# Optimization experiments

Measured on AMD Instinct MI355X. Metric: run time of the kernel, lower is better.

## Reference

```python
import jax, jax.numpy as jnp
import numpy as np

B, T, C = 2, 2048, 2048
NH, NKV = 16, 4
HD = C // NH  # 128
DFF = 4 * C


def rmsnorm(x):
    eps = jnp.finfo(x.dtype).eps
    return x * jax.lax.rsqrt(jnp.mean(jnp.square(x), axis=-1, keepdims=True) + eps)


def rotary(x, cos, sin):
    # x: [B,T,H,HD], cos/sin: [1,T,1,HD//2]
    d = x.shape[-1] // 2
    x1, x2 = x[..., :d], x[..., d:]
    return jnp.concatenate([x1 * cos + x2 * sin, -x1 * sin + x2 * cos], axis=-1)


def setup_inputs() -> dict:
    key = jax.random.key(0)
    ks = jax.random.split(key, 8)
    x = jax.random.normal(ks[0], (B, T, C), jnp.float32)
    inv_freq = 1.0 / (10000.0 ** (jnp.arange(HD // 2, dtype=jnp.float32) / (HD // 2)))
    ang = jnp.arange(T, dtype=jnp.float32)[:, None] * inv_freq[None, :]  # [T, HD//2]
    cos = jnp.cos(ang)[None, :, None, :]
    sin = jnp.sin(ang)[None, :, None, :]
    s = 0.02
    wq = jax.random.normal(ks[1], (C, NH * HD), jnp.float32) * s
    wk = jax.random.normal(ks[2], (C, NKV * HD), jnp.float32) * s
    wv = jax.random.normal(ks[3], (C, NKV * HD), jnp.float32) * s
    wo = jax.random.normal(ks[4], (C, C), jnp.float32) * s
    w_fc = jax.random.normal(ks[5], (C, DFF), jnp.float32) * s
    w_proj = jax.random.normal(ks[6], (DFF, C), jnp.float32) * s
    return {"x": x, "cos": cos, "sin": sin, "wq": wq, "wk": wk, "wv": wv,
            "wo": wo, "w_fc": w_fc, "w_proj": w_proj}


def reference(x, cos, sin, wq, wk, wv, wo, w_fc, w_proj):
    # --- attention sublayer (pre-norm residual) ---
    h = rmsnorm(x)
    q = (h @ wq).reshape(B, T, NH, HD)
    k = (h @ wk).reshape(B, T, NKV, HD)
    v = (h @ wv).reshape(B, T, NKV, HD)
    q = rmsnorm(rotary(q, cos, sin))
    k = rmsnorm(rotary(k, cos, sin))
    rep = NH // NKV
    k = jnp.repeat(k, rep, axis=2)  # [B,T,NH,HD]
    v = jnp.repeat(v, rep, axis=2)
    scale = 1.0 / np.sqrt(HD)
    scores = jnp.einsum('bqhd,bkhd->bhqk', q, k) * scale
    causal = jnp.tril(jnp.ones((T, T), dtype=bool))
    scores = jnp.where(causal[None, None], scores, jnp.finfo(scores.dtype).min)
    attn = jax.nn.softmax(scores, axis=-1)
    y = jnp.einsum('bhqk,bkhd->bqhd', attn, v).reshape(B, T, C)
    x = x + y @ wo
    # --- MLP sublayer (relu^2) ---
    h = rmsnorm(x)
    h = jnp.square(jax.nn.relu(h @ w_fc))
    x = x + h @ w_proj
    return x
```

## Files before the change

kernel.cpp:

```cpp
#include <hip/hip_runtime.h>
#include <cstdint>
#include <cstddef>


#define B_    2
#define T_    2048
#define C_    2048
#define NH_   16
#define NKV_  4
#define HD_   128
#define DFF_  8192
#define EPS_  1.1920928955078125e-07f

typedef short          bf16x8 __attribute__((ext_vector_type(8)));
typedef float          f32x4  __attribute__((ext_vector_type(4)));
typedef unsigned short u16;
typedef unsigned short u16x8  __attribute__((ext_vector_type(8)));
typedef unsigned short u16x4  __attribute__((ext_vector_type(4)));

__device__ __forceinline__ u16 f2bf(float f) {
    unsigned u = __float_as_uint(f);
    unsigned r = u + 0x7fffu + ((u >> 16) & 1u);
    return (u16)(r >> 16);
}
__device__ __forceinline__ float bf2f(u16 u) {
    return __uint_as_float((unsigned)u << 16);
}

__device__ __forceinline__ void load_lds16(const void* g, void* l) {
    __builtin_amdgcn_global_load_lds(
        (__attribute__((address_space(1))) void*)(g),
        (__attribute__((address_space(3))) void*)(l), 16, 0, 0);
}

__device__ __forceinline__ unsigned lds_addr(const void* p) {
    return (unsigned)(unsigned long long)(__attribute__((address_space(3))) const void*)p;
}

struct TD  { const float* src; u16* dst; int K, N, boff; };
struct TD6 { TD t[6]; };

#define TRBLKS_ 10752

__global__ void prep_all(TD6 d, const float* __restrict__ x, u16* __restrict__ hout) {
    __shared__ u16 tile[32][136];
    __shared__ float part[4];
    int bid = blockIdx.x;
    int tid = threadIdx.x;

    if (bid >= TRBLKS_) {
        int row = bid - TRBLKS_;
        const float4* xr = (const float4*)(x + (size_t)row * C_);
        float4 a = xr[tid];
        float4 b = xr[tid + 256];
        float ss = a.x * a.x + a.y * a.y + a.z * a.z + a.w * a.w
                 + b.x * b.x + b.y * b.y + b.z * b.z + b.w * b.w;
        for (int m = 1; m < 64; m <<= 1) ss += __shfl_xor(ss, m, 64);
        if ((tid & 63) == 0) part[tid >> 6] = ss;
        __syncthreads();
        float tot = part[0] + part[1] + part[2] + part[3];
        float sc = rsqrtf(tot * (1.0f / C_) + EPS_);
        u16x4 o1, o2;
        o1[0] = f2bf(a.x * sc); o1[1] = f2bf(a.y * sc); o1[2] = f2bf(a.z * sc); o1[3] = f2bf(a.w * sc);
        o2[0] = f2bf(b.x * sc); o2[1] = f2bf(b.y * sc); o2[2] = f2bf(b.z * sc); o2[3] = f2bf(b.w * sc);
        u16x4* orow = (u16x4*)(hout + (size_t)row * C_);
        orow[tid]       = o1;
        orow[tid + 256] = o2;
        return;
    }

    int di = 0;
    for (int i = 5; i > 0; --i) if (bid >= d.t[i].boff) { di = i; break; }
    const float* src = d.t[di].src;
    u16* dst = d.t[di].dst;
    int K = d.t[di].K, N = d.t[di].N;
    int lb = bid - d.t[di].boff;
    int nx = N >> 5;
    int n0 = (lb % nx) * 32;
    int k0 = (lb / nx) * 128;

    int kr = tid >> 3;
    int nc = (tid & 7) * 4;
    for (int r = 0; r < 4; ++r) {
        int kk = kr + r * 32;
        float4 v = *(const float4*)&src[(size_t)(k0 + kk) * N + n0 + nc];
        tile[nc + 0][kk] = f2bf(v.x);
        tile[nc + 1][kk] = f2bf(v.y);
        tile[nc + 2][kk] = f2bf(v.z);
        tile[nc + 3][kk] = f2bf(v.w);
    }
    __syncthreads();
    int nL = tid >> 4;
    int kc = (tid & 15) * 8;
    for (int w2 = 0; w2 < 2; ++w2) {
        int n = nL + w2 * 16;
        u16x8 o = *(const u16x8*)&tile[n][kc];
        *(u16x8*)&dst[(size_t)(n0 + n) * K + k0 + kc] = o;
    }
}

#define TVB_ 1024

__global__ void rope_tv(const float* __restrict__ Xq, const float* __restrict__ Xk,
                        const float* __restrict__ cosb, const float* __restrict__ sinb,
                        u16* __restrict__ Oq, u16* __restrict__ Ok,
                        const u16* __restrict__ vb, u16* __restrict__ Vt) {
    int bid = blockIdx.x;
    if (bid < TVB_) {
        int bxx  = bid & 127;
        int kvh  = (bid >> 7) & 3;
        int b    = bid >> 9;
        int dblk = bxx & 1;
        int t0   = (bxx >> 1) * 32;
        int dl   = threadIdx.x & 63;
        int tc   = threadIdx.x >> 6;
        int d    = dblk * 64 + dl;
        u16x8 v8;
        for (int j = 0; j < 8; ++j) {
            int t = t0 + tc * 8 + j;
            v8[j] = vb[((size_t)(b * T_ + t) * NKV_ + kvh) * HD_ + d];
        }
        *(u16x8*)(Vt + ((size_t)((b * NKV_ + kvh) * HD_ + d)) * T_ + t0 + tc * 8) = v8;
        return;
    }
    int gw   = (int)(((bid - TVB_) * blockDim.x + threadIdx.x) >> 6);
    int lane = threadIdx.x & 63;
    const float* X; u16* O; int t;
    if (gw < B_ * T_ * NH_) {
        X = Xq + (size_t)gw * HD_;  O = Oq + (size_t)gw * HD_;  t = (gw / NH_) % T_;
    } else {
        int w2 = gw - B_ * T_ * NH_;
        X = Xk + (size_t)w2 * HD_;  O = Ok + (size_t)w2 * HD_;  t = (w2 / NKV_) % T_;
    }
    float x1 = X[lane];
    float x2 = X[64 + lane];
    float c  = cosb[t * 64 + lane];
    float sn = sinb[t * 64 + lane];
    float r1 = x1 * c + x2 * sn;
    float r2 = x2 * c - x1 * sn;
    float ss = r1 * r1 + r2 * r2;
    for (int m = 1; m < 64; m <<= 1) ss += __shfl_xor(ss, m, 64);
    float sc = rsqrtf(ss * (1.0f / HD_) + EPS_);
    O[lane]      = f2bf(r1 * sc);
    O[64 + lane] = f2bf(r2 * sc);
}

__global__ void reduce_rms(const float* __restrict__ x, const u16* __restrict__ p0,
                           const u16* __restrict__ p1, float* __restrict__ x2,
                           u16* __restrict__ hout) {
    int row = blockIdx.x;
    const float4* xr = (const float4*)(x + (size_t)row * C_);
    const u16x4* a0 = (const u16x4*)(p0 + (size_t)row * C_);
    const u16x4* a1 = (const u16x4*)(p1 + (size_t)row * C_);
    float4 v[2];
    float ss = 0.f;
    for (int h = 0; h < 2; ++h) {
        int idx = threadIdx.x + h * 256;
        float4 xv = xr[idx];
        u16x4 b0 = a0[idx], b1 = a1[idx];
        v[h].x = xv.x + bf2f(b0[0]) + bf2f(b1[0]);
        v[h].y = xv.y + bf2f(b0[1]) + bf2f(b1[1]);
        v[h].z = xv.z + bf2f(b0[2]) + bf2f(b1[2]);
        v[h].w = xv.w + bf2f(b0[3]) + bf2f(b1[3]);
        ss += v[h].x * v[h].x + v[h].y * v[h].y + v[h].z * v[h].z + v[h].w * v[h].w;
    }
    for (int m = 1; m < 64; m <<= 1) ss += __shfl_xor(ss, m, 64);
    __shared__ float part[4];
    if ((threadIdx.x & 63) == 0) part[threadIdx.x >> 6] = ss;
    __syncthreads();
    float tot = part[0] + part[1] + part[2] + part[3];
    float sc = rsqrtf(tot * (1.0f / C_) + EPS_);
    float4* x2r = (float4*)(x2 + (size_t)row * C_);
    u16x4* hr   = (u16x4*)(hout + (size_t)row * C_);
    for (int h = 0; h < 2; ++h) {
        int idx = threadIdx.x + h * 256;
        x2r[idx] = v[h];
        u16x4 o;
        o[0] = f2bf(v[h].x * sc); o[1] = f2bf(v[h].y * sc);
        o[2] = f2bf(v[h].z * sc); o[3] = f2bf(v[h].w * sc);
        hr[idx] = o;
    }
}

__global__ void reduce_out(const float* __restrict__ x2, const u16* __restrict__ p0,
                           const u16* __restrict__ p1, float* __restrict__ out) {
    size_t i = (size_t)blockIdx.x * 256 + threadIdx.x;
    float4 xv = ((const float4*)x2)[i];
    u16x4 b0 = ((const u16x4*)p0)[i];
    u16x4 b1 = ((const u16x4*)p1)[i];
    float4 o;
    o.x = xv.x + bf2f(b0[0]) + bf2f(b1[0]);
    o.y = xv.y + bf2f(b0[1]) + bf2f(b1[1]);
    o.z = xv.z + bf2f(b0[2]) + bf2f(b1[2]);
    o.w = xv.w + bf2f(b0[3]) + bf2f(b1[3]);
    ((float4*)out)[i] = o;
}


#define BARRIER() do { __builtin_amdgcn_s_barrier();                     \
                       asm volatile("" ::: "memory"); } while (0)
#define LGKMN(N)  do { asm volatile("s_waitcnt lgkmcnt(" #N ")" ::: "memory");\
                       __builtin_amdgcn_sched_barrier(0); } while (0)

#define DSR(dst, base, lit)                                              \
    asm volatile("ds_read_b128 %0, %1 offset:" lit : "=v"(dst) : "v"(base))

#define READ_AFL() do {                                                  \
    DSR(afl[0][0], aB0, "0");     DSR(afl[0][1], aB1, "0");              \
    DSR(afl[1][0], aB0, "2048");  DSR(afl[1][1], aB1, "2048");           \
    DSR(afl[2][0], aB0, "4096");  DSR(afl[2][1], aB1, "4096");           \
    DSR(afl[3][0], aB0, "6144");  DSR(afl[3][1], aB1, "6144"); } while (0)

#define READ_AFH() do {                                                  \
    DSR(afh[0][0], aB0, "8192");  DSR(afh[0][1], aB1, "8192");           \
    DSR(afh[1][0], aB0, "10240"); DSR(afh[1][1], aB1, "10240");          \
    DSR(afh[2][0], aB0, "12288"); DSR(afh[2][1], aB1, "12288");          \
    DSR(afh[3][0], aB0, "14336"); DSR(afh[3][1], aB1, "14336"); } while (0)

#define READ_BL() do {                                                   \
    DSR(bl[0][0], bB0, "0");     DSR(bl[0][1], bB1, "0");                \
    DSR(bl[1][0], bB0, "2048");  DSR(bl[1][1], bB1, "2048"); } while (0)

#define READ_BH() do {                                                   \
    DSR(bh[0][0], bB0, "4096");  DSR(bh[0][1], bB1, "4096");             \
    DSR(bh[1][0], bB0, "6144");  DSR(bh[1][1], bB1, "6144"); } while (0)

#define MFMA_BLK(AF, BF, MB, NB)                                             \
    _Pragma("unroll")                                                        \
    for (int ks = 0; ks < 2; ++ks)                                           \
        _Pragma("unroll")                                                    \
        for (int mi = 0; mi < 4; ++mi)                                       \
            _Pragma("unroll")                                                \
            for (int ni = 0; ni < 2; ++ni)                                   \
                acc[MB + mi][NB + ni] =                                      \
                    __builtin_amdgcn_mfma_f32_16x16x32_bf16(                 \
                        AF[mi][ks], BF[ni][ks], acc[MB + mi][NB + ni], 0, 0, 0);

template <int EPI>
__launch_bounds__(512, 1)
__global__ void gemm256(const u16* __restrict__ A, const u16* __restrict__ Bt,
                        void* __restrict__ out, void* __restrict__ out2,
                        void* __restrict__ out3, int M, int N, int K, int Ks) {
    __shared__ __attribute__((aligned(16))) u16 sh[65536];

    int tid  = threadIdx.x;
    int l    = tid & 63;
    int w    = tid >> 6;
    int l16  = l & 15;
    int quad = l >> 4;
    int sw   = l & 7;
    int wm   = w >> 2, wn = w & 3;

    int nwg = gridDim.x * gridDim.y;
    int id  = blockIdx.y * gridDim.x + blockIdx.x;
    int cpx = nwg >> 3;
    int sid = (id & 7) * cpx + (id >> 3);
    int GN   = (cpx >= 64) ? 8 : 4;
    int span = gridDim.y * GN;
    int bnb  = sid / span;
    int r0   = sid % span;
    int bm   = r0 / GN;
    int bn   = bnb * GN + (r0 % GN);

    size_t koff = (size_t)blockIdx.z * K;
    int nt = K >> 6;

    int csrc = ((l & 7) ^ ((l >> 3) & 7)) * 8;
    int srow = w * 8 + (l >> 3);
    const u16* Ast = A  + (size_t)(bm * 256 + srow) * Ks + koff + csrc;
    const u16* Bst = Bt + (size_t)(bn * 256 + srow) * Ks + koff + csrc;

    auto stageA = [&](int h, int kk, int buf) {
        const u16* g = Ast + (size_t)(h * 128) * Ks + kk;
        u16* d = sh + buf * 32768 + h * 8192 + w * 512;
        load_lds16(g, d);
        load_lds16(g + (size_t)64 * Ks, d + 4096);
    };
    auto stageB = [&](int h, int kk, int buf) {
        const u16* g = Bst + (size_t)(h * 128) * Ks + kk;
        u16* d = sh + buf * 32768 + (2 + h) * 8192 + w * 512;
        load_lds16(g, d);
        load_lds16(g + (size_t)64 * Ks, d + 4096);
    };

    f32x4 acc[8][4];
#pragma unroll
    for (int m = 0; m < 8; ++m)
#pragma unroll
        for (int n = 0; n < 4; ++n) acc[m][n] = (f32x4){0.f, 0.f, 0.f, 0.f};

    stageB(0, 0, 0); stageA(0, 0, 0); stageA(1, 0, 0); stageB(1, 0, 0);
    stageB(0, 64, 1); stageA(0, 64, 1);
    asm volatile("s_waitcnt vmcnt(4)" ::: "memory");
    BARRIER();

    bf16x8 afl[4][2], afh[4][2], bl[2][2], bh[2][2];
    unsigned shbase = lds_addr(sh);
    unsigned ck0 = (unsigned)((quad ^ sw) * 16);
    unsigned ck1 = ck0 ^ 64u;
    unsigned Aoff = (unsigned)(wm * 16384 + l16 * 128);
    unsigned Boff = (unsigned)((2 + (wn >> 1)) * 16384 + (wn & 1) * 8192
                               + l16 * 128);
    unsigned aB0c = shbase + Aoff + ck0, aB1c = shbase + Aoff + ck1;
    unsigned bB0c = shbase + Boff + ck0, bB1c = shbase + Boff + ck1;

    for (int t = 0; t < nt; ++t) {
        int buf = t & 1;
        unsigned bo  = (unsigned)buf << 16;
        unsigned aB0 = aB0c + bo, aB1 = aB1c + bo;
        unsigned bB0 = bB0c + bo, bB1 = bB1c + bo;
        bool s1 = (t + 1 < nt), s2 = (t + 2 < nt);

        READ_AFL();
        READ_BL();
        READ_BH();
        READ_AFH();
        if (s1) { stageA(1, (t + 1) * 64, buf ^ 1);
                  stageB(1, (t + 1) * 64, buf ^ 1); }

        LGKMN(12);
        __builtin_amdgcn_s_setprio(1);
        MFMA_BLK(afl, bl, 0, 0);
        __builtin_amdgcn_s_setprio(0);

        LGKMN(8);
        __builtin_amdgcn_s_setprio(1);
        MFMA_BLK(afl, bh, 0, 2);
        __builtin_amdgcn_s_setprio(0);

        LGKMN(0);
        BARRIER();
        if (s2) { stageB(0, (t + 2) * 64, buf);
                  stageA(0, (t + 2) * 64, buf); }

        __builtin_amdgcn_s_setprio(1);
        MFMA_BLK(afh, bl, 4, 0);
        MFMA_BLK(afh, bh, 4, 2);
        __builtin_amdgcn_s_setprio(0);

        if (s2)      asm volatile("s_waitcnt vmcnt(4)" ::: "memory");
        else if (s1) asm volatile("s_waitcnt vmcnt(0)" ::: "memory");
        BARRIER();
    }

#pragma unroll
    for (int m = 0; m < 8; ++m)
#pragma unroll
        for (int n = 0; n < 4; ++n)
#pragma unroll
            for (int r = 0; r < 4; ++r) {
                int rg = bm * 256 + wm * 128 + m * 16 + quad * 4 + r;
                int cg = bn * 256 + wn * 64 + n * 16 + l16;
                float v = acc[m][n][r];
                if (EPI == 2) {
                    float tv = fmaxf(v, 0.f);
                    ((u16*)out)[(size_t)rg * N + cg] = f2bf(tv * tv);
                } else if (EPI == 4) {
                    if (cg < 2048)      ((float*)out)[(size_t)rg * 2048 + cg] = v;
                    else if (cg < 2560) ((float*)out2)[(size_t)rg * 512 + (cg - 2048)] = v;
                    else                ((u16*)out3)[(size_t)rg * 512 + (cg - 2560)] = f2bf(v);
                } else {
                    u16* p = (blockIdx.z == 0) ? (u16*)out : (u16*)out2;
                    p[(size_t)rg * N + cg] = f2bf(v);
                }
            }
}

__launch_bounds__(256, 2)
__global__ void flash_attn2(const u16* __restrict__ Q, const u16* __restrict__ Kb,
                            const u16* __restrict__ Vt, u16* __restrict__ Y) {
    __shared__ __attribute__((aligned(16))) u16 Qs[128 * 128];
    __shared__ __attribute__((aligned(16))) u16 Ks[64 * 128];
    __shared__ __attribute__((aligned(16))) u16 Vs[2][128 * 64];

    int bid = blockIdx.x;
    int half = bid >> 8, idx = bid & 255;
    int qr = idx & 15;
    int qt = half ? (15 - qr) : qr;
    int bh = (idx >> 4) | (half << 4);
    int b = bh >> 4, h = bh & 15;
    int kvh = h >> 2;
    int q0 = qt * 128;

    int tid = threadIdx.x, lane = tid & 63, wave = tid >> 6;
    int quad = lane >> 4, l16 = lane & 15;

    {
        int r = lane >> 4;
        for (int c = 0; c < 8; ++c) {
            int row = wave * 32 + c * 4 + r;
            int cc = ((lane & 15) ^ (row & 15)) * 8;
            const u16* g = Q + ((size_t)((b * T_ + q0 + row) * NH_ + h)) * HD_ + cc;
            load_lds16(g, &Qs[(wave * 32 + c * 4) * 128]);
        }
    }
    __syncthreads();

    bf16x8 qf[2][4];
    for (int qtile = 0; qtile < 2; ++qtile)
        for (int kd = 0; kd < 4; ++kd)
            qf[qtile][kd] = *(const bf16x8*)&Qs[(wave * 32 + qtile * 16 + l16) * 128
                                               + (((kd * 4 + quad) ^ l16) * 8)];
    u16* Ps = &Qs[wave * 32 * 128];

    auto stageK = [&](int kt) {
        int r = lane >> 4;
        for (int c = 0; c < 4; ++c) {
            int row = wave * 16 + c * 4 + r;
            int cc = ((lane & 15) ^ (row & 15)) * 8;
            const u16* g = Kb + ((size_t)((b * T_ + kt * 64 + row) * NKV_ + kvh)) * HD_ + cc;
            load_lds16(g, &Ks[(wave * 16 + c * 4) * 128]);
        }
    };
    auto stageV = [&](int kt, int vb) {
        int dr = lane >> 3;
        int kc = (((lane & 7) ^ dr)) * 8;
        for (int c = 0; c < 4; ++c) {
            int drow = wave * 32 + c * 8 + dr;
            const u16* g = Vt + ((size_t)((b * NKV_ + kvh) * HD_ + drow)) * T_ + kt * 64 + kc;
            load_lds16(g, &Vs[vb][(wave * 32 + c * 8) * 64]);
        }
    };

    f32x4 zero = {0.f, 0.f, 0.f, 0.f};
    f32x4 o[2][8];
    for (int qtile = 0; qtile < 2; ++qtile)
        for (int dt = 0; dt < 8; ++dt) o[qtile][dt] = zero;
    float m_i[2] = {-__builtin_inff(), -__builtin_inff()};
    float l_i[2] = {0.f, 0.f};
    const float s2s = 0.08838834764831845f * 1.4426950408889634f;

    int nkt = 2 * qt + 2;
    stageK(0); stageV(0, 0);

    for (int kt = 0; kt < nkt; ++kt) {
        int vcur = kt & 1;
        __syncthreads();

        f32x4 st[2][4];
        for (int qtile = 0; qtile < 2; ++qtile)
            for (int tn = 0; tn < 4; ++tn) st[qtile][tn] = zero;
        __builtin_amdgcn_s_setprio(1);
        for (int tn = 0; tn < 4; ++tn)
            for (int kd = 0; kd < 4; ++kd) {
                bf16x8 kf = *(const bf16x8*)&Ks[(tn * 16 + l16) * 128
                                                + (((kd * 4 + quad) ^ l16) * 8)];
                st[0][tn] = __builtin_amdgcn_mfma_f32_16x16x32_bf16(kf, qf[0][kd], st[0][tn], 0, 0, 0);
                st[1][tn] = __builtin_amdgcn_mfma_f32_16x16x32_bf16(kf, qf[1][kd], st[1][tn], 0, 0, 0);
            }
        __builtin_amdgcn_s_setprio(0);

        __syncthreads();
        if (kt + 1 < nkt) {
            stageK(kt + 1);
            stageV(kt + 1, vcur ^ 1);
        }

        for (int qtile = 0; qtile < 2; ++qtile) {
            int qmin = q0 + wave * 32 + qtile * 16;
            int qg   = qmin + l16;
            bool need_mask = (kt * 64 + 63 > qmin);
            float mx = -__builtin_inff();
            for (int tn = 0; tn < 4; ++tn)
                for (int r = 0; r < 4; ++r) {
                    float v = st[qtile][tn][r] * s2s;
                    if (need_mask) {
                        int key = kt * 64 + tn * 16 + quad * 4 + r;
                        if (key > qg) v = -__builtin_inff();
                    }
                    st[qtile][tn][r] = v;
                    mx = fmaxf(mx, v);
                }
            mx = fmaxf(mx, __shfl_xor(mx, 16, 64));
            mx = fmaxf(mx, __shfl_xor(mx, 32, 64));
            float mnew = fmaxf(m_i[qtile], mx);
            float al   = exp2f(m_i[qtile] - mnew);
            m_i[qtile] = mnew;
            float sum = 0.f;
            for (int tn = 0; tn < 4; ++tn) {
                u16x4 pk;
                for (int r = 0; r < 4; ++r) {
                    float e = exp2f(st[qtile][tn][r] - mnew);
                    sum += e;
                    pk[r] = f2bf(e);
                }
                *(u16x4*)&Ps[(qtile * 16 + l16) * 72 + tn * 16 + quad * 4] = pk;
            }
            sum += __shfl_xor(sum, 16, 64);
            sum += __shfl_xor(sum, 32, 64);
            l_i[qtile] = l_i[qtile] * al + sum;
            float aB[4];
            for (int r = 0; r < 4; ++r) aB[r] = __shfl(al, quad * 4 + r, 64);
            for (int dt = 0; dt < 8; ++dt)
                for (int r = 0; r < 4; ++r) o[qtile][dt][r] *= aB[r];
        }

        bf16x8 pf[2][2];
        for (int qtile = 0; qtile < 2; ++qtile)
            for (int ks = 0; ks < 2; ++ks)
                pf[qtile][ks] = *(const bf16x8*)&Ps[(qtile * 16 + l16) * 72 + ks * 32 + quad * 8];
        __builtin_amdgcn_s_setprio(1);
        for (int ks = 0; ks < 2; ++ks)
            for (int dt = 0; dt < 8; ++dt) {
                bf16x8 vf = *(const bf16x8*)&Vs[vcur][(dt * 16 + l16) * 64
                                                + (((ks * 4 + quad) ^ (l16 & 7)) * 8)];
                o[0][dt] = __builtin_amdgcn_mfma_f32_16x16x32_bf16(pf[0][ks], vf, o[0][dt], 0, 0, 0);
                o[1][dt] = __builtin_amdgcn_mfma_f32_16x16x32_bf16(pf[1][ks], vf, o[1][dt], 0, 0, 0);
            }
        __builtin_amdgcn_s_setprio(0);
    }

    for (int qtile = 0; qtile < 2; ++qtile) {
        float inv = 1.0f / l_i[qtile];
        float iB[4];
        for (int r = 0; r < 4; ++r) iB[r] = __shfl(inv, quad * 4 + r, 64);
        for (int r = 0; r < 4; ++r) {
            int qg = q0 + wave * 32 + qtile * 16 + quad * 4 + r;
            u16* yr = Y + ((size_t)((b * T_ + qg) * NH_ + h)) * HD_;
            for (int dt = 0; dt < 8; ++dt)
                yr[dt * 16 + l16] = f2bf(o[qtile][dt][r] * iB[r]);
        }
    }
}

extern "C" void kernel_launch(void* const* d_in, const int* in_sizes, int n_in,
                              void* d_out, int out_size, void* d_ws, size_t ws_size,
                              hipStream_t stream) {
    const float* x     = (const float*)d_in[0];
    const float* cosb  = (const float*)d_in[1];
    const float* sinb  = (const float*)d_in[2];
    const float* wq    = (const float*)d_in[3];
    const float* wk    = (const float*)d_in[4];
    const float* wv    = (const float*)d_in[5];
    const float* wo    = (const float*)d_in[6];
    const float* wfc   = (const float*)d_in[7];
    const float* wproj = (const float*)d_in[8];

    char* ws = (char*)d_ws;
    size_t off = 0;
    auto alloc = [&](size_t bytes) { char* p = ws + off; off += (bytes + 255) & ~(size_t)255; return p; };

    u16*   wqkvT  = (u16*)alloc((size_t)3072 * C_ * 2);
    u16*   woT    = (u16*)alloc((size_t)C_ * C_ * 2);
    u16*   wfcT   = (u16*)alloc((size_t)DFF_ * C_ * 2);
    u16*   wprojT = (u16*)alloc((size_t)C_ * DFF_ * 2);
    u16*   hbuf   = (u16*)alloc((size_t)B_ * T_ * C_ * 2);
    float* x2     = (float*)alloc((size_t)B_ * T_ * C_ * 4);
    u16*   ybuf   = (u16*)alloc((size_t)B_ * T_ * C_ * 2);
    u16*   Vtb    = (u16*)alloc((size_t)B_ * NKV_ * HD_ * T_ * 2);
    char*  scratch = alloc((size_t)B_ * T_ * DFF_ * 2);
    float* q_tmp  = (float*)scratch;
    float* k_tmp  = (float*)(scratch + (size_t)B_ * T_ * C_ * 4);
    u16*   qb     = (u16*)(scratch + (size_t)B_ * T_ * C_ * 4 + (size_t)B_ * T_ * 512 * 4);
    u16*   kb     = (u16*)((char*)qb + (size_t)B_ * T_ * C_ * 2);
    u16*   vb     = (u16*)((char*)kb + (size_t)B_ * T_ * 512 * 2);
    u16*   wop1   = (u16*)scratch;
    u16*   ffbuf  = (u16*)scratch;

    const int M = B_ * T_;
    dim3 tb(256);

    TD6 td;
    td.t[0] = { wq,    wqkvT,                       C_,   C_,   0 };
    td.t[1] = { wk,    wqkvT + (size_t)2048 * C_,   C_,   512,  1024 };
    td.t[2] = { wv,    wqkvT + (size_t)2560 * C_,   C_,   512,  1280 };
    td.t[3] = { wo,    woT,                         C_,   C_,   1536 };
    td.t[4] = { wfc,   wfcT,                        C_,   DFF_, 2560 };
    td.t[5] = { wproj, wprojT,                      DFF_, C_,   6656 };
    prep_all<<<dim3(TRBLKS_ + M), tb, 0, stream>>>(td, x, hbuf);

    gemm256<4><<<dim3(3072 / 256, M / 256), dim3(512), 0, stream>>>(
        hbuf, wqkvT, q_tmp, k_tmp, vb, M, 3072, C_, C_);

    rope_tv<<<dim3(TVB_ + (B_ * T_ * (NH_ + NKV_)) / 4), tb, 0, stream>>>(
        q_tmp, k_tmp, cosb, sinb, qb, kb, vb, Vtb);

    flash_attn2<<<dim3(512), tb, 0, stream>>>(qb, kb, Vtb, ybuf);

    gemm256<5><<<dim3(C_ / 256, M / 256, 2), dim3(512), 0, stream>>>(
        ybuf, woT, hbuf, wop1, nullptr, M, C_, C_ / 2, C_);

    reduce_rms<<<M, tb, 0, stream>>>(x, hbuf, wop1, x2, hbuf);

    gemm256<2><<<dim3(DFF_ / 256, M / 256), dim3(512), 0, stream>>>(
        hbuf, wfcT, ffbuf, nullptr, nullptr, M, DFF_, C_, C_);

    gemm256<5><<<dim3(C_ / 256, M / 256, 2), dim3(512), 0, stream>>>(
        ffbuf, wprojT, hbuf, ybuf, nullptr, M, C_, DFF_ / 2, DFF_);

    reduce_out<<<dim3((M * C_) / 1024), tb, 0, stream>>>(x2, hbuf, ybuf, (float*)d_out);
}
```

Before: 694.2 us.

## Prefetch next-tile LDS fragments in GEMM and lazily rescale attention accumulators

In the 256x256 GEMM main loop, the low A and B fragments for the next k-tile are now read from LDS right after the end-of-iteration barrier. The last MFMA block is moved after those reads so it overlaps with their latency, and the prologue issues the first fragment reads before the loop. In the flash-attention softmax, the running max and output rescale are updated only when some row's new max exceeds the old one by more than 8 (in log2 units), skipping exp2 and the accumulator multiplies otherwise. The lazy rescale makes exponentials up to 2^8 larger before normalisation. It also puts a lane shuffle inside a branch that can diverge per lane, which is a correctness risk.

```diff
diff --git a/kernel.cpp b/kernel.cpp
--- a/kernel.cpp
+++ b/kernel.cpp
@@ -205,25 +205,25 @@
 #define DSR(dst, base, lit)                                              \
     asm volatile("ds_read_b128 %0, %1 offset:" lit : "=v"(dst) : "v"(base))
 
-#define READ_AFL() do {                                                  \
-    DSR(afl[0][0], aB0, "0");     DSR(afl[0][1], aB1, "0");              \
-    DSR(afl[1][0], aB0, "2048");  DSR(afl[1][1], aB1, "2048");           \
-    DSR(afl[2][0], aB0, "4096");  DSR(afl[2][1], aB1, "4096");           \
-    DSR(afl[3][0], aB0, "6144");  DSR(afl[3][1], aB1, "6144"); } while (0)
-
-#define READ_AFH() do {                                                  \
-    DSR(afh[0][0], aB0, "8192");  DSR(afh[0][1], aB1, "8192");           \
-    DSR(afh[1][0], aB0, "10240"); DSR(afh[1][1], aB1, "10240");          \
-    DSR(afh[2][0], aB0, "12288"); DSR(afh[2][1], aB1, "12288");          \
-    DSR(afh[3][0], aB0, "14336"); DSR(afh[3][1], aB1, "14336"); } while (0)
-
-#define READ_BL() do {                                                   \
-    DSR(bl[0][0], bB0, "0");     DSR(bl[0][1], bB1, "0");                \
-    DSR(bl[1][0], bB0, "2048");  DSR(bl[1][1], bB1, "2048"); } while (0)
-
-#define READ_BH() do {                                                   \
-    DSR(bh[0][0], bB0, "4096");  DSR(bh[0][1], bB1, "4096");             \
-    DSR(bh[1][0], bB0, "6144");  DSR(bh[1][1], bB1, "6144"); } while (0)
+#define READ_AFL(a0, a1) do {                                            \
+    DSR(afl[0][0], a0, "0");     DSR(afl[0][1], a1, "0");                \
+    DSR(afl[1][0], a0, "2048");  DSR(afl[1][1], a1, "2048");             \
+    DSR(afl[2][0], a0, "4096");  DSR(afl[2][1], a1, "4096");             \
+    DSR(afl[3][0], a0, "6144");  DSR(afl[3][1], a1, "6144"); } while (0)
+
+#define READ_AFH(a0, a1) do {                                            \
+    DSR(afh[0][0], a0, "8192");  DSR(afh[0][1], a1, "8192");             \
+    DSR(afh[1][0], a0, "10240"); DSR(afh[1][1], a1, "10240");            \
+    DSR(afh[2][0], a0, "12288"); DSR(afh[2][1], a1, "12288");            \
+    DSR(afh[3][0], a0, "14336"); DSR(afh[3][1], a1, "14336"); } while (0)
+
+#define READ_BL(b0, b1) do {                                             \
+    DSR(bl[0][0], b0, "0");     DSR(bl[0][1], b1, "0");                  \
+    DSR(bl[1][0], b0, "2048");  DSR(bl[1][1], b1, "2048"); } while (0)
+
+#define READ_BH(b0, b1) do {                                             \
+    DSR(bh[0][0], b0, "4096");  DSR(bh[0][1], b1, "4096");               \
+    DSR(bh[1][0], b0, "6144");  DSR(bh[1][1], b1, "6144"); } while (0)
 
 #define MFMA_BLK(AF, BF, MB, NB)                                             \
     _Pragma("unroll")                                                        \
@@ -289,11 +289,6 @@
 #pragma unroll
         for (int n = 0; n < 4; ++n) acc[m][n] = (f32x4){0.f, 0.f, 0.f, 0.f};
 
-    stageB(0, 0, 0); stageA(0, 0, 0); stageA(1, 0, 0); stageB(1, 0, 0);
-    stageB(0, 64, 1); stageA(0, 64, 1);
-    asm volatile("s_waitcnt vmcnt(4)" ::: "memory");
-    BARRIER();
-
     bf16x8 afl[4][2], afh[4][2], bl[2][2], bh[2][2];
     unsigned shbase = lds_addr(sh);
     unsigned ck0 = (unsigned)((quad ^ sw) * 16);
@@ -304,17 +299,23 @@
     unsigned aB0c = shbase + Aoff + ck0, aB1c = shbase + Aoff + ck1;
     unsigned bB0c = shbase + Boff + ck0, bB1c = shbase + Boff + ck1;
 
+    stageB(0, 0, 0); stageA(0, 0, 0); stageA(1, 0, 0); stageB(1, 0, 0);
+    stageB(0, 64, 1); stageA(0, 64, 1);
+    asm volatile("s_waitcnt vmcnt(4)" ::: "memory");
+    BARRIER();
+    READ_BL(bB0c, bB1c);
+    READ_AFL(aB0c, aB1c);
+
     for (int t = 0; t < nt; ++t) {
         int buf = t & 1;
         unsigned bo  = (unsigned)buf << 16;
+        unsigned nbo = (unsigned)(buf ^ 1) << 16;
         unsigned aB0 = aB0c + bo, aB1 = aB1c + bo;
         unsigned bB0 = bB0c + bo, bB1 = bB1c + bo;
         bool s1 = (t + 1 < nt), s2 = (t + 2 < nt);
 
-        READ_AFL();
-        READ_BL();
-        READ_BH();
-        READ_AFH();
+        READ_BH(bB0, bB1);
+        READ_AFH(aB0, aB1);
         if (s1) { stageA(1, (t + 1) * 64, buf ^ 1);
                   stageB(1, (t + 1) * 64, buf ^ 1); }
 
@@ -335,12 +336,20 @@
 
         __builtin_amdgcn_s_setprio(1);
         MFMA_BLK(afh, bl, 4, 0);
-        MFMA_BLK(afh, bh, 4, 2);
         __builtin_amdgcn_s_setprio(0);
 
         if (s2)      asm volatile("s_waitcnt vmcnt(4)" ::: "memory");
         else if (s1) asm volatile("s_waitcnt vmcnt(0)" ::: "memory");
         BARRIER();
+
+        if (s1) {
+            READ_BL(bB0c + nbo, bB1c + nbo);
+            READ_AFL(aB0c + nbo, aB1c + nbo);
+        }
+
+        __builtin_amdgcn_s_setprio(1);
+        MFMA_BLK(afh, bh, 4, 2);
+        __builtin_amdgcn_s_setprio(0);
     }
 
 #pragma unroll
@@ -473,14 +482,18 @@
                 }
             mx = fmaxf(mx, __shfl_xor(mx, 16, 64));
             mx = fmaxf(mx, __shfl_xor(mx, 32, 64));
-            float mnew = fmaxf(m_i[qtile], mx);
-            float al   = exp2f(m_i[qtile] - mnew);
-            m_i[qtile] = mnew;
+            float al = 1.0f;
+            if (!__all(mx - m_i[qtile] <= 8.0f)) {
+                float mnew = fmaxf(m_i[qtile], mx);
+                al = exp2f(m_i[qtile] - mnew);
+                m_i[qtile] = mnew;
+            }
+            float mref = m_i[qtile];
             float sum = 0.f;
             for (int tn = 0; tn < 4; ++tn) {
                 u16x4 pk;
                 for (int r = 0; r < 4; ++r) {
-                    float e = exp2f(st[qtile][tn][r] - mnew);
+                    float e = exp2f(st[qtile][tn][r] - mref);
                     sum += e;
                     pk[r] = f2bf(e);
                 }
@@ -489,10 +502,12 @@
             sum += __shfl_xor(sum, 16, 64);
             sum += __shfl_xor(sum, 32, 64);
             l_i[qtile] = l_i[qtile] * al + sum;
-            float aB[4];
-            for (int r = 0; r < 4; ++r) aB[r] = __shfl(al, quad * 4 + r, 64);
-            for (int dt = 0; dt < 8; ++dt)
-                for (int r = 0; r < 4; ++r) o[qtile][dt][r] *= aB[r];
+            if (al != 1.0f) {
+                float aB[4];
+                for (int r = 0; r < 4; ++r) aB[r] = __shfl(al, quad * 4 + r, 64);
+                for (int dt = 0; dt < 8; ++dt)
+                    for (int r = 0; r < 4; ++r) o[qtile][dt][r] *= aB[r];
+            }
         }
 
         bf16x8 pf[2][2];
```

Result: slower. 805.0 us (+16.0%).
